# Kernel tuning notes

Measured on AMD Instinct MI355X. Metric: run time of the kernel, lower is better.

The kernel has to match this reference:

```python
import jax, jax.numpy as jnp
import numpy as np

N_NODES = 50000
N_EDGES = 800000
F_IN = 128
NUM_GRAPHS = 64
BN_EPS = 1e-5


def _graph_conv(x, src, dst, ew, Wl, bl, Wr, n_nodes):
    # PyG GraphConv: out = lin_l(aggr_add(x_j * w_e)) + lin_r(x)
    msg = x[src] * ew[:, None]                       # [E, F]
    agg = jax.ops.segment_sum(msg, dst, num_segments=n_nodes)  # [N, F]
    return agg @ Wl + bl + x @ Wr


def setup_inputs() -> dict:
    key = jax.random.key(0)
    ks = jax.random.split(key, 16)
    x = jax.random.normal(ks[0], (N_NODES, F_IN), dtype=jnp.float32)
    edge_index = jax.random.randint(ks[1], (2, N_EDGES), 0, N_NODES, dtype=jnp.int64)
    edge_attr = jax.random.uniform(ks[2], (N_EDGES,), dtype=jnp.float32)
    batch = jnp.sort(jax.random.randint(ks[3], (N_NODES,), 0, NUM_GRAPHS, dtype=jnp.int64))

    def lin(k, fin, fout):
        s = 1.0 / np.sqrt(fin)
        return jax.random.uniform(k, (fin, fout), jnp.float32, -s, s)

    params = {
        "Wl1": lin(ks[4], F_IN, 512), "bl1": jnp.zeros((512,), jnp.float32), "Wr1": lin(ks[5], F_IN, 512),
        "Wl2": lin(ks[6], 512, 512),  "bl2": jnp.zeros((512,), jnp.float32), "Wr2": lin(ks[7], 512, 512),
        "Wl3": lin(ks[8], 512, 256),  "bl3": jnp.zeros((256,), jnp.float32), "Wr3": lin(ks[9], 512, 256),
        "bn_gamma": jnp.ones((512,), jnp.float32), "bn_beta": jnp.zeros((512,), jnp.float32),
        "bn_mean": jnp.zeros((512,), jnp.float32),  "bn_var": jnp.ones((512,), jnp.float32),
        "W4": lin(ks[10], 256, 64), "b4": jnp.zeros((64,), jnp.float32),
        "W5": lin(ks[11], 64, 1),  "b5": jnp.zeros((1,), jnp.float32),
    }
    return {"x": x, "edge_index": edge_index, "edge_attr": edge_attr, "batch": batch, **params}


def reference(x, edge_index, edge_attr, batch,
              Wl1, bl1, Wr1, Wl2, bl2, Wr2, Wl3, bl3, Wr3,
              bn_gamma, bn_beta, bn_mean, bn_var,
              W4, b4, W5, b5):
    src, dst = edge_index[0], edge_index[1]
    n = x.shape[0]
    h = jax.nn.relu(_graph_conv(x, src, dst, edge_attr, Wl1, bl1, Wr1, n))
    h = _graph_conv(h, src, dst, edge_attr, Wl2, bl2, Wr2, n)
    # BatchNorm1d in eval mode (running stats)
    h = (h - bn_mean) * jax.lax.rsqrt(bn_var + BN_EPS) * bn_gamma + bn_beta
    h = jax.nn.relu(h)
    h = jax.nn.relu(_graph_conv(h, src, dst, edge_attr, Wl3, bl3, Wr3, n))
    # global mean pool
    sums = jax.ops.segment_sum(h, batch, num_segments=NUM_GRAPHS)           # [G, 256]
    cnts = jax.ops.segment_sum(jnp.ones((n,), h.dtype), batch, num_segments=NUM_GRAPHS)
    g = sums / jnp.maximum(cnts, 1.0)[:, None]
    # dropout is identity in eval mode
    g = jax.nn.relu(g @ W4 + b4)
    return jax.nn.relu(g @ W5 + b5)  # [G, 1]
```

## Files before the change

kernel.cpp:

```cpp
#include <hip/hip_runtime.h>

#define NN 50000
#define NE 800000
#define NG 64
#define BN_EPS 1e-5f

typedef unsigned short u16;
typedef unsigned int u32;
typedef unsigned char u8;
typedef long i64b;
struct alignas(8) us4 { u16 x, y, z, w; };
typedef float f32x4 __attribute__((ext_vector_type(4)));

__device__ inline int clampi(int v, int lo, int hi) {
  return v < lo ? lo : (v > hi ? hi : v);
}
__device__ inline float bf2f(u16 h) { return __uint_as_float((u32)h << 16); }
__device__ inline u16 f2bf_rne(float f) {
  u32 u = __float_as_uint(f);
  return (u16)((u + 0x7fff + ((u >> 16) & 1)) >> 16);
}
__device__ inline void gload_lds16(const void* g, void* l) {
  __builtin_amdgcn_global_load_lds(
      (const __attribute__((address_space(1))) u32*)g,
      (__attribute__((address_space(3))) u32*)l, 16, 0, 0);
}
__device__ inline float4 fp8x4f(u32 q) {
  float4 r;
  r.x = __builtin_amdgcn_cvt_f32_fp8(q, 0);
  r.y = __builtin_amdgcn_cvt_f32_fp8(q, 1);
  r.z = __builtin_amdgcn_cvt_f32_fp8(q, 2);
  r.w = __builtin_amdgcn_cvt_f32_fp8(q, 3);
  return r;
}
__device__ inline u32 f4fp8(float a, float b, float c, float d) {
  u32 p = __builtin_amdgcn_cvt_pk_fp8_f32(a, b, 0u, false);
  return __builtin_amdgcn_cvt_pk_fp8_f32(c, d, p, true);
}
__device__ inline u8 f2fp8(float v) {
  return (u8)(__builtin_amdgcn_cvt_pk_fp8_f32(v, 0.f, 0u, false) & 0xffu);
}

__global__ void k_zero32(u32* __restrict__ p, int n) {
  int i = blockIdx.x * 256 + threadIdx.x;
  if (i < n) p[i] = 0u;
}

__global__ void k_count(const int* __restrict__ dst, int* __restrict__ deg) {
  int e = blockIdx.x * 256 + threadIdx.x;
  if (e < NE) atomicAdd(&deg[clampi(dst[e], 0, NN - 1)], 1);
}

__global__ void k_scan_block(const int* __restrict__ deg, int* __restrict__ excl,
                             int* __restrict__ aux) {
  __shared__ int s[256];
  int t = threadIdx.x;
  int idx = blockIdx.x * 256 + t;
  int v = (idx < NN) ? deg[idx] : 0;
  s[t] = v;
  __syncthreads();
  for (int off = 1; off < 256; off <<= 1) {
    int x = (t >= off) ? s[t - off] : 0;
    __syncthreads();
    s[t] += x;
    __syncthreads();
  }
  if (idx < NN) excl[idx] = s[t] - v;
  if (t == 255) aux[blockIdx.x] = s[255];
}

__global__ void k_scan_aux(int* aux, int nblk) {
  __shared__ int s[256];
  int t = threadIdx.x;
  int v = (t < nblk) ? aux[t] : 0;
  s[t] = v;
  __syncthreads();
  for (int off = 1; off < 256; off <<= 1) {
    int x = (t >= off) ? s[t - off] : 0;
    __syncthreads();
    s[t] += x;
    __syncthreads();
  }
  if (t < nblk) aux[t] = s[t] - v;
}

__global__ void k_fix(int* __restrict__ rowptr, const int* __restrict__ aux,
                      int* __restrict__ cursor) {
  int idx = blockIdx.x * 256 + threadIdx.x;
  if (idx < NN) {
    int v = rowptr[idx] + aux[blockIdx.x];
    rowptr[idx] = v;
    cursor[idx] = v;
  }
  if (idx == 0) rowptr[NN] = NE;
}

__global__ void k_fill(const int* __restrict__ src, const int* __restrict__ dst,
                       const float* __restrict__ ew, int* __restrict__ cursor,
                       int* __restrict__ csr_src, float* __restrict__ csr_w) {
  int e = blockIdx.x * 256 + threadIdx.x;
  if (e < NE) {
    int d = clampi(dst[e], 0, NN - 1);
    int p = atomicAdd(&cursor[d], 1);
    p = clampi(p, 0, NE - 1);
    csr_src[p] = clampi(src[e], 0, NN - 1);
    csr_w[p] = ew[e];
  }
}

__global__ void k_prep(const float* __restrict__ x, u8* __restrict__ xf8,
                       const float* __restrict__ Wl1, const float* __restrict__ Wr1,
                       u8* __restrict__ t1,
                       const float* __restrict__ Wl2, const float* __restrict__ Wr2,
                       u8* __restrict__ t2,
                       const float* __restrict__ Wl3, const float* __restrict__ Wr3,
                       u8* __restrict__ t3) {
  int b = blockIdx.x, tid = threadIdx.x;
  if (b < 512) {
    int n = b, k = tid;
    float v = (k < 128) ? Wl1[(size_t)k * 512 + n] : Wr1[(size_t)(k - 128) * 512 + n];
    t1[(size_t)n * 256 + k] = f2fp8(v);
  } else if (b < 1024) {
    int n = b - 512;
    for (int k = tid; k < 1024; k += 256) {
      float v = (k < 512) ? Wl2[(size_t)k * 512 + n] : Wr2[(size_t)(k - 512) * 512 + n];
      t2[(size_t)n * 1024 + k] = f2fp8(v);
    }
  } else if (b < 1536) {
    int n = b - 1024;
    for (int k = tid; k < 512; k += 256) {
      float v = (n < 256) ? Wl3[(size_t)k * 256 + n] : Wr3[(size_t)k * 256 + (n - 256)];
      t3[(size_t)n * 512 + k] = f2fp8(v);
    }
  } else {
    int i = (b - 1536) * 256 + tid;
    if (i < NN * 128 / 8) {
      size_t o = (size_t)i * 8;
      float4 a = *(const float4*)(x + o);
      float4 c = *(const float4*)(x + o + 4);
      u32 p0 = f4fp8(a.x, a.y, a.z, a.w);
      u32 p1 = f4fp8(c.x, c.y, c.z, c.w);
      *(uint2*)(xf8 + o) = make_uint2(p0, p1);
    }
  }
}

__global__ void k_aggf512(const u8* __restrict__ xf8, const int* __restrict__ rowptr,
                          const int* __restrict__ csr_src, const float* __restrict__ csr_w,
                          u8* __restrict__ out) {
  int n = blockIdx.x;
  int t = threadIdx.x;
  int beg = rowptr[n], end = rowptr[n + 1];
  float4 acc = {0.f, 0.f, 0.f, 0.f};
  int e = beg;
  for (; e + 4 <= end; e += 4) {
    int s0 = csr_src[e], s1 = csr_src[e + 1];
    int s2 = csr_src[e + 2], s3 = csr_src[e + 3];
    float w0 = csr_w[e], w1 = csr_w[e + 1];
    float w2 = csr_w[e + 2], w3 = csr_w[e + 3];
    u32 q0 = *(const u32*)(xf8 + (size_t)s0 * 512 + t * 4);
    u32 q1 = *(const u32*)(xf8 + (size_t)s1 * 512 + t * 4);
    u32 q2 = *(const u32*)(xf8 + (size_t)s2 * 512 + t * 4);
    u32 q3 = *(const u32*)(xf8 + (size_t)s3 * 512 + t * 4);
    float4 v0 = fp8x4f(q0), v1 = fp8x4f(q1), v2 = fp8x4f(q2), v3 = fp8x4f(q3);
    acc.x += v0.x * w0 + v1.x * w1 + v2.x * w2 + v3.x * w3;
    acc.y += v0.y * w0 + v1.y * w1 + v2.y * w2 + v3.y * w3;
    acc.z += v0.z * w0 + v1.z * w1 + v2.z * w2 + v3.z * w3;
    acc.w += v0.w * w0 + v1.w * w1 + v2.w * w2 + v3.w * w3;
  }
  for (; e < end; ++e) {
    int s0 = csr_src[e];
    float w0 = csr_w[e];
    float4 v0 = fp8x4f(*(const u32*)(xf8 + (size_t)s0 * 512 + t * 4));
    acc.x += v0.x * w0; acc.y += v0.y * w0;
    acc.z += v0.z * w0; acc.w += v0.w * w0;
  }
  *(u32*)(out + (size_t)n * 512 + t * 4) = f4fp8(acc.x, acc.y, acc.z, acc.w);
}

__global__ void k_aggf128(const u8* __restrict__ xf8, const int* __restrict__ rowptr,
                          const int* __restrict__ csr_src, const float* __restrict__ csr_w,
                          u8* __restrict__ out) {
  int sub = threadIdx.x >> 5;
  int lane = threadIdx.x & 31;
  int n = blockIdx.x * 2 + sub;
  if (n >= NN) return;
  int beg = rowptr[n], end = rowptr[n + 1];
  float4 acc = {0.f, 0.f, 0.f, 0.f};
  int e = beg;
  for (; e + 2 <= end; e += 2) {
    int s0 = csr_src[e], s1 = csr_src[e + 1];
    float w0 = csr_w[e], w1 = csr_w[e + 1];
    float4 v0 = fp8x4f(*(const u32*)(xf8 + (size_t)s0 * 128 + lane * 4));
    float4 v1 = fp8x4f(*(const u32*)(xf8 + (size_t)s1 * 128 + lane * 4));
    acc.x += v0.x * w0 + v1.x * w1;
    acc.y += v0.y * w0 + v1.y * w1;
    acc.z += v0.z * w0 + v1.z * w1;
    acc.w += v0.w * w0 + v1.w * w1;
  }
  if (e < end) {
    int s0 = csr_src[e];
    float w0 = csr_w[e];
    float4 v0 = fp8x4f(*(const u32*)(xf8 + (size_t)s0 * 128 + lane * 4));
    acc.x += v0.x * w0; acc.y += v0.y * w0;
    acc.z += v0.z * w0; acc.w += v0.w * w0;
  }
  *(u32*)(out + (size_t)n * 128 + lane * 4) = f4fp8(acc.x, acc.y, acc.z, acc.w);
}

__global__ void k_aggcomb(const u8* __restrict__ P, const u8* __restrict__ Q,
                          const int* __restrict__ rowptr, const int* __restrict__ csr_src,
                          const float* __restrict__ csr_w,
                          const float* __restrict__ bl3, u16* __restrict__ h3) {
  int sub = threadIdx.x >> 6;
  int lane = threadIdx.x & 63;
  int n = blockIdx.x * 2 + sub;
  if (n >= NN) return;
  int beg = rowptr[n], end = rowptr[n + 1];
  float4 acc = {0.f, 0.f, 0.f, 0.f};
  int e = beg;
  for (; e + 4 <= end; e += 4) {
    int s0 = csr_src[e], s1 = csr_src[e + 1];
    int s2 = csr_src[e + 2], s3 = csr_src[e + 3];
    float w0 = csr_w[e], w1 = csr_w[e + 1];
    float w2 = csr_w[e + 2], w3 = csr_w[e + 3];
    float4 v0 = fp8x4f(*(const u32*)(P + (size_t)s0 * 256 + lane * 4));
    float4 v1 = fp8x4f(*(const u32*)(P + (size_t)s1 * 256 + lane * 4));
    float4 v2 = fp8x4f(*(const u32*)(P + (size_t)s2 * 256 + lane * 4));
    float4 v3 = fp8x4f(*(const u32*)(P + (size_t)s3 * 256 + lane * 4));
    acc.x += v0.x * w0 + v1.x * w1 + v2.x * w2 + v3.x * w3;
    acc.y += v0.y * w0 + v1.y * w1 + v2.y * w2 + v3.y * w3;
    acc.z += v0.z * w0 + v1.z * w1 + v2.z * w2 + v3.z * w3;
    acc.w += v0.w * w0 + v1.w * w1 + v2.w * w2 + v3.w * w3;
  }
  for (; e < end; ++e) {
    int s0 = csr_src[e];
    float w0 = csr_w[e];
    float4 v0 = fp8x4f(*(const u32*)(P + (size_t)s0 * 256 + lane * 4));
    acc.x += v0.x * w0; acc.y += v0.y * w0;
    acc.z += v0.z * w0; acc.w += v0.w * w0;
  }
  float4 qv = fp8x4f(*(const u32*)(Q + (size_t)n * 256 + lane * 4));
  float4 bb = *(const float4*)(bl3 + lane * 4);
  us4 o;
  o.x = f2bf_rne(fmaxf(acc.x + qv.x + bb.x, 0.f));
  o.y = f2bf_rne(fmaxf(acc.y + qv.y + bb.y, 0.f));
  o.z = f2bf_rne(fmaxf(acc.z + qv.z + bb.z, 0.f));
  o.w = f2bf_rne(fmaxf(acc.w + qv.w + bb.w, 0.f));
  *(us4*)(h3 + (size_t)n * 256 + lane * 4) = o;
}

template <int K, int W0, int EPI>
__global__ __launch_bounds__(256) void k_gemm(
    const u8* __restrict__ A0, const u8* __restrict__ A1,
    const u8* __restrict__ Wt, const float* __restrict__ bias,
    const float* __restrict__ gamma, const float* __restrict__ beta,
    const float* __restrict__ mean, const float* __restrict__ var,
    u8* __restrict__ O8g, u8* __restrict__ O8b) {
  constexpr int FOUT = 512;
  __shared__ char LDSC[32768];
  u8* AS = (u8*)LDSC;
  u8* BS = (u8*)(LDSC + 16384);
  int tid = threadIdx.x;
  int wid = tid >> 6, l = tid & 63;
  int wr = wid >> 1, wc = wid & 1;

  int nwg = gridDim.x;
  int q8 = nwg >> 3, r8 = nwg & 7;
  int xcd = blockIdx.x & 7, idx = blockIdx.x >> 3;
  int L = (xcd < r8 ? xcd * (q8 + 1) : r8 * (q8 + 1) + (xcd - r8) * q8) + idx;
  int n0 = (L >> 2) * 128, c0 = (L & 3) * 128;

  f32x4 acc[4][4] = {};

  int srw = 32 * wid + (l >> 3);
  int sch = l & 7;

  for (int k0 = 0; k0 < K; k0 += 128) {
    __syncthreads();
    {
      const u8* s; int rs; int seg;
      if (k0 < W0) { s = A0; rs = W0; seg = k0; }
      else         { s = A1; rs = K - W0; seg = k0 - W0; }
#pragma unroll
      for (int j = 0; j < 4; ++j) {
        int r = srw + 8 * j;
        int gr = n0 + r;
        if (gr >= NN) gr = NN - 1;
        int cc = sch ^ (r & 7);
        gload_lds16(s + (size_t)gr * rs + seg + cc * 16, AS + (32 * wid + 8 * j) * 128);
      }
#pragma unroll
      for (int j = 0; j < 4; ++j) {
        int r = srw + 8 * j;
        int cc = sch ^ (r & 7);
        gload_lds16(Wt + (size_t)(c0 + r) * K + k0 + cc * 16, BS + (32 * wid + 8 * j) * 128);
      }
    }
    __syncthreads();

#pragma unroll
    for (int ks = 0; ks < 4; ++ks) {
      i64b b[4];
#pragma unroll
      for (int n = 0; n < 4; ++n) {
        int col = wc * 64 + n * 16 + (l & 15);
        int byte = (col * 128 + ks * 32 + ((l >> 4) << 3)) ^ ((col & 7) << 4);
        b[n] = *(const i64b*)((const char*)BS + byte);
      }
#pragma unroll
      for (int m = 0; m < 4; ++m) {
        int row = wr * 64 + m * 16 + (l & 15);
        int byte = (row * 128 + ks * 32 + ((l >> 4) << 3)) ^ ((row & 7) << 4);
        i64b a = *(const i64b*)((const char*)AS + byte);
#pragma unroll
        for (int n = 0; n < 4; ++n)
          acc[m][n] = __builtin_amdgcn_mfma_f32_16x16x32_fp8_fp8(a, b[n], acc[m][n], 0, 0, 0);
      }
    }
  }

  __syncthreads();
  u8* O8 = (u8*)LDSC;
#pragma unroll
  for (int n = 0; n < 4; ++n) {
    int colL = wc * 64 + n * 16 + (l & 15);
    int col = c0 + colL;
    float bs = (EPI == 2) ? 0.f : bias[col];
    float sc = 1.f, sf = 0.f;
    if (EPI == 1) {
      sc = rsqrtf(var[col] + BN_EPS) * gamma[col];
      sf = beta[col] - mean[col] * sc;
    }
#pragma unroll
    for (int m = 0; m < 4; ++m) {
      int rowL0 = wr * 64 + m * 16 + ((l >> 4) << 2);
#pragma unroll
      for (int r = 0; r < 4; ++r) {
        float v = acc[m][n][r];
        if (EPI != 2) {
          v += bs;
          if (EPI == 1) v = v * sc + sf;
          v = fmaxf(v, 0.f);
        }
        int rowL = rowL0 + r;
        int byte = (rowL * 128 + colL) ^ ((rowL & 7) << 4);
        O8[byte] = f2fp8(v);
      }
    }
  }
  __syncthreads();
#pragma unroll
  for (int i = 0; i < 4; ++i) {
    int chunk = i * 256 + tid;
    int rowL = chunk >> 3;
    int cs = (chunk & 7) * 16;
    int rr = n0 + rowL;
    if (rr < NN) {
      int byte = (rowL * 128 + cs) ^ ((rowL & 7) << 4);
      uint4 val = *(const uint4*)((const char*)O8 + byte);
      if (EPI == 2) {
        u8* dstp = (c0 < 256) ? O8g : O8b;
        int cc0 = (c0 < 256) ? c0 : c0 - 256;
        *(uint4*)(dstp + (size_t)rr * 256 + cc0 + cs) = val;
      } else {
        *(uint4*)(O8g + (size_t)rr * FOUT + c0 + cs) = val;
      }
    }
  }
}

__global__ void k_counts(const int* __restrict__ batch, float* __restrict__ cnt) {
  int g = threadIdx.x;
  int lo = 0, hi = NN;
  while (lo < hi) { int m = (lo + hi) >> 1; if (batch[m] < g) lo = m + 1; else hi = m; }
  int a = lo;
  lo = 0; hi = NN;
  int g1 = g + 1;
  while (lo < hi) { int m = (lo + hi) >> 1; if (batch[m] < g1) lo = m + 1; else hi = m; }
  cnt[g] = (float)(lo - a);
}

__global__ void k_pool(const u16* __restrict__ h, const int* __restrict__ batch,
                       float* __restrict__ sums) {
  int f = threadIdx.x;
  int n0 = blockIdx.x * 128;
  int n1 = n0 + 128; if (n1 > NN) n1 = NN;
  float acc = 0.f;
  int cur = clampi(batch[n0], 0, NG - 1);
  for (int n = n0; n < n1; ++n) {
    int g = clampi(batch[n], 0, NG - 1);
    if (g != cur) {
      atomicAdd(&sums[(size_t)cur * 256 + f], acc);
      acc = 0.f;
      cur = g;
    }
    acc += bf2f(h[(size_t)n * 256 + f]);
  }
  atomicAdd(&sums[(size_t)cur * 256 + f], acc);
}

__global__ void k_mlp(const float* __restrict__ sums, const float* __restrict__ cnt,
                      const float* __restrict__ W4, const float* __restrict__ b4,
                      const float* __restrict__ W5, const float* __restrict__ b5,
                      float* __restrict__ out) {
  __shared__ float g[256];
  int b = blockIdx.x, t = threadIdx.x;
  float inv = 1.f / fmaxf(cnt[b], 1.f);
#pragma unroll
  for (int q = 0; q < 4; ++q) g[q * 64 + t] = sums[(size_t)b * 256 + q * 64 + t] * inv;
  __syncthreads();
  float acc = 0.f;
#pragma unroll 8
  for (int k = 0; k < 256; ++k) acc += g[k] * W4[k * 64 + t];
  float a = fmaxf(acc + b4[t], 0.f) * W5[t];
  for (int off = 32; off; off >>= 1) a += __shfl_down(a, off, 64);
  if (t == 0) out[b] = fmaxf(a + b5[0], 0.f);
}

extern "C" void kernel_launch(void* const* d_in, const int* in_sizes, int n_in,
                              void* d_out, int out_size, void* d_ws, size_t ws_size,
                              hipStream_t stream) {
  const float* x     = (const float*)d_in[0];
  const int*   eidx  = (const int*)d_in[1];
  const float* ew    = (const float*)d_in[2];
  const int*   batch = (const int*)d_in[3];
  const float* Wl1 = (const float*)d_in[4];
  const float* bl1 = (const float*)d_in[5];
  const float* Wr1 = (const float*)d_in[6];
  const float* Wl2 = (const float*)d_in[7];
  const float* bl2 = (const float*)d_in[8];
  const float* Wr2 = (const float*)d_in[9];
  const float* Wl3 = (const float*)d_in[10];
  const float* bl3 = (const float*)d_in[11];
  const float* Wr3 = (const float*)d_in[12];
  const float* gamma = (const float*)d_in[13];
  const float* beta  = (const float*)d_in[14];
  const float* mean  = (const float*)d_in[15];
  const float* var   = (const float*)d_in[16];
  const float* W4 = (const float*)d_in[17];
  const float* b4 = (const float*)d_in[18];
  const float* W5 = (const float*)d_in[19];
  const float* b5 = (const float*)d_in[20];

  const int* src = eidx;
  const int* dst = eidx + NE;

  const size_t P8 = (size_t)NN * 512;
  char* w = (char*)d_ws;
  u8*  X1f8 = (u8*)w; w += P8;
  u8*  X2f8 = (u8*)w; w += P8;
  u8*  Agf8 = (u8*)w; w += P8;
  u8*  Xf8  = (u8*)w; w += (size_t)NN * 128;
  u16* h3 = (u16*)w; w += (size_t)NN * 256 * 2;
  u8* Wt1 = (u8*)w; w += (size_t)512 * 256;
  u8* Wt2 = (u8*)w; w += (size_t)512 * 1024;
  u8* Wt3 = (u8*)w; w += (size_t)512 * 512;
  int*   csr_src = (int*)w;   w += (size_t)NE * 4;
  float* csr_w   = (float*)w; w += (size_t)NE * 4;
  int*   rowptr  = (int*)w;   w += ((size_t)NN + 4) * 4;
  int*   cursor  = (int*)w;   w += (size_t)NN * 4;
  int*   aux     = (int*)w;   w += 1024;
  float* sums    = (float*)w; w += (size_t)NG * 256 * 4;
  float* cnt     = (float*)w; w += 1024;
  u8* Pf8 = Agf8;
  u8* Qf8 = Agf8 + (size_t)NN * 256;

  int nblk = (NN + 255) / 256;

  k_zero32<<<nblk, 256, 0, stream>>>((u32*)cursor, NN);
  k_count<<<(NE + 255) / 256, 256, 0, stream>>>(dst, cursor);
  k_scan_block<<<nblk, 256, 0, stream>>>(cursor, rowptr, aux);
  k_scan_aux<<<1, 256, 0, stream>>>(aux, nblk);
  k_fix<<<nblk, 256, 0, stream>>>(rowptr, aux, cursor);
  k_fill<<<(NE + 255) / 256, 256, 0, stream>>>(src, dst, ew, cursor, csr_src, csr_w);
  k_prep<<<1536 + (NN * 128 / 8 + 255) / 256, 256, 0, stream>>>(
      x, Xf8, Wl1, Wr1, Wt1, Wl2, Wr2, Wt2, Wl3, Wr3, Wt3);

  const int NWG = 391 * 4;

  k_aggf128<<<(NN + 1) / 2, 64, 0, stream>>>(Xf8, rowptr, csr_src, csr_w, Agf8);
  k_gemm<256, 128, 0><<<NWG, 256, 0, stream>>>(
      Agf8, Xf8, Wt1, bl1, nullptr, nullptr, nullptr, nullptr, X1f8, nullptr);

  k_aggf512<<<NN, 128, 0, stream>>>(X1f8, rowptr, csr_src, csr_w, Agf8);
  k_gemm<1024, 512, 1><<<NWG, 256, 0, stream>>>(
      Agf8, X1f8, Wt2, bl2, gamma, beta, mean, var, X2f8, nullptr);

  k_gemm<512, 512, 2><<<NWG, 256, 0, stream>>>(
      X2f8, X2f8, Wt3, nullptr, nullptr, nullptr, nullptr, nullptr, Pf8, Qf8);
  k_aggcomb<<<(NN + 1) / 2, 128, 0, stream>>>(Pf8, Qf8, rowptr, csr_src, csr_w, bl3, h3);

  k_zero32<<<(NG * 256 + 255) / 256, 256, 0, stream>>>((u32*)sums, NG * 256);
  k_pool<<<(NN + 127) / 128, 256, 0, stream>>>(h3, batch, sums);
  k_counts<<<1, 64, 0, stream>>>(batch, cnt);
  k_mlp<<<NG, 64, 0, stream>>>(sums, cnt, W4, b4, W5, b5, (float*)d_out);
}
```

Measured before the change: 402.7 us.

## Fuse pooling, counts and MLP; pack two nodes per aggf512 block; unroll aggf128

Replaces the zero, pool, count and MLP kernels with one fused kernel, one block per graph. Each block binary-searches its node range, sums the h3 rows in a serial loop, then runs the small MLP. This removes three launches and the atomics. k_aggf512 now handles two nodes per 256-thread block, and k_aggf128 unrolls its edge loop by four for more loads in flight. The risk is that only 64 blocks each walk about 780 rows serially, so the pooling step may become latency-bound with little parallelism.

```diff
diff --git a/kernel.cpp b/kernel.cpp
--- a/kernel.cpp
+++ b/kernel.cpp
@@ -148,8 +148,10 @@
 __global__ void k_aggf512(const u8* __restrict__ xf8, const int* __restrict__ rowptr,
                           const int* __restrict__ csr_src, const float* __restrict__ csr_w,
                           u8* __restrict__ out) {
-  int n = blockIdx.x;
-  int t = threadIdx.x;
+  int sub = threadIdx.x >> 7;
+  int t = threadIdx.x & 127;
+  int n = blockIdx.x * 2 + sub;
+  if (n >= NN) return;
   int beg = rowptr[n], end = rowptr[n + 1];
   float4 acc = {0.f, 0.f, 0.f, 0.f};
   int e = beg;
@@ -188,17 +190,21 @@
   int beg = rowptr[n], end = rowptr[n + 1];
   float4 acc = {0.f, 0.f, 0.f, 0.f};
   int e = beg;
-  for (; e + 2 <= end; e += 2) {
+  for (; e + 4 <= end; e += 4) {
     int s0 = csr_src[e], s1 = csr_src[e + 1];
+    int s2 = csr_src[e + 2], s3 = csr_src[e + 3];
     float w0 = csr_w[e], w1 = csr_w[e + 1];
+    float w2 = csr_w[e + 2], w3 = csr_w[e + 3];
     float4 v0 = fp8x4f(*(const u32*)(xf8 + (size_t)s0 * 128 + lane * 4));
     float4 v1 = fp8x4f(*(const u32*)(xf8 + (size_t)s1 * 128 + lane * 4));
-    acc.x += v0.x * w0 + v1.x * w1;
-    acc.y += v0.y * w0 + v1.y * w1;
-    acc.z += v0.z * w0 + v1.z * w1;
-    acc.w += v0.w * w0 + v1.w * w1;
-  }
-  if (e < end) {
+    float4 v2 = fp8x4f(*(const u32*)(xf8 + (size_t)s2 * 128 + lane * 4));
+    float4 v3 = fp8x4f(*(const u32*)(xf8 + (size_t)s3 * 128 + lane * 4));
+    acc.x += v0.x * w0 + v1.x * w1 + v2.x * w2 + v3.x * w3;
+    acc.y += v0.y * w0 + v1.y * w1 + v2.y * w2 + v3.y * w3;
+    acc.z += v0.z * w0 + v1.z * w1 + v2.z * w2 + v3.z * w3;
+    acc.w += v0.w * w0 + v1.w * w1 + v2.w * w2 + v3.w * w3;
+  }
+  for (; e < end; ++e) {
     int s0 = csr_src[e];
     float w0 = csr_w[e];
     float4 v0 = fp8x4f(*(const u32*)(xf8 + (size_t)s0 * 128 + lane * 4));
@@ -370,52 +376,31 @@
   }
 }
 
-__global__ void k_counts(const int* __restrict__ batch, float* __restrict__ cnt) {
-  int g = threadIdx.x;
-  int lo = 0, hi = NN;
-  while (lo < hi) { int m = (lo + hi) >> 1; if (batch[m] < g) lo = m + 1; else hi = m; }
-  int a = lo;
-  lo = 0; hi = NN;
-  int g1 = g + 1;
-  while (lo < hi) { int m = (lo + hi) >> 1; if (batch[m] < g1) lo = m + 1; else hi = m; }
-  cnt[g] = (float)(lo - a);
-}
-
-__global__ void k_pool(const u16* __restrict__ h, const int* __restrict__ batch,
-                       float* __restrict__ sums) {
-  int f = threadIdx.x;
-  int n0 = blockIdx.x * 128;
-  int n1 = n0 + 128; if (n1 > NN) n1 = NN;
-  float acc = 0.f;
-  int cur = clampi(batch[n0], 0, NG - 1);
-  for (int n = n0; n < n1; ++n) {
-    int g = clampi(batch[n], 0, NG - 1);
-    if (g != cur) {
-      atomicAdd(&sums[(size_t)cur * 256 + f], acc);
-      acc = 0.f;
-      cur = g;
-    }
-    acc += bf2f(h[(size_t)n * 256 + f]);
-  }
-  atomicAdd(&sums[(size_t)cur * 256 + f], acc);
-}
-
-__global__ void k_mlp(const float* __restrict__ sums, const float* __restrict__ cnt,
-                      const float* __restrict__ W4, const float* __restrict__ b4,
-                      const float* __restrict__ W5, const float* __restrict__ b5,
-                      float* __restrict__ out) {
+__global__ void k_poolmlp(const u16* __restrict__ h3, const int* __restrict__ batch,
+                          const float* __restrict__ W4, const float* __restrict__ b4,
+                          const float* __restrict__ W5, const float* __restrict__ b5,
+                          float* __restrict__ out) {
   __shared__ float g[256];
   int b = blockIdx.x, t = threadIdx.x;
-  float inv = 1.f / fmaxf(cnt[b], 1.f);
-#pragma unroll
-  for (int q = 0; q < 4; ++q) g[q * 64 + t] = sums[(size_t)b * 256 + q * 64 + t] * inv;
+  int lo = 0, hi = NN;
+  while (lo < hi) { int m = (lo + hi) >> 1; if (batch[m] < b) lo = m + 1; else hi = m; }
+  int a0 = lo;
+  lo = 0; hi = NN;
+  int b1 = b + 1;
+  while (lo < hi) { int m = (lo + hi) >> 1; if (batch[m] < b1) lo = m + 1; else hi = m; }
+  int a1 = lo;
+  float acc = 0.f;
+  for (int n = a0; n < a1; ++n) acc += bf2f(h3[(size_t)n * 256 + t]);
+  g[t] = acc / fmaxf((float)(a1 - a0), 1.f);
   __syncthreads();
-  float acc = 0.f;
+  if (t < 64) {
+    float s = 0.f;
 #pragma unroll 8
-  for (int k = 0; k < 256; ++k) acc += g[k] * W4[k * 64 + t];
-  float a = fmaxf(acc + b4[t], 0.f) * W5[t];
-  for (int off = 32; off; off >>= 1) a += __shfl_down(a, off, 64);
-  if (t == 0) out[b] = fmaxf(a + b5[0], 0.f);
+    for (int k = 0; k < 256; ++k) s += g[k] * W4[k * 64 + t];
+    float a = fmaxf(s + b4[t], 0.f) * W5[t];
+    for (int off = 32; off; off >>= 1) a += __shfl_down(a, off, 64);
+    if (t == 0) out[b] = fmaxf(a + b5[0], 0.f);
+  }
 }
 
 extern "C" void kernel_launch(void* const* d_in, const int* in_sizes, int n_in,
@@ -461,8 +446,6 @@
   int*   rowptr  = (int*)w;   w += ((size_t)NN + 4) * 4;
   int*   cursor  = (int*)w;   w += (size_t)NN * 4;
   int*   aux     = (int*)w;   w += 1024;
-  float* sums    = (float*)w; w += (size_t)NG * 256 * 4;
-  float* cnt     = (float*)w; w += 1024;
   u8* Pf8 = Agf8;
   u8* Qf8 = Agf8 + (size_t)NN * 256;
 
@@ -483,7 +466,7 @@
   k_gemm<256, 128, 0><<<NWG, 256, 0, stream>>>(
       Agf8, Xf8, Wt1, bl1, nullptr, nullptr, nullptr, nullptr, X1f8, nullptr);
 
-  k_aggf512<<<NN, 128, 0, stream>>>(X1f8, rowptr, csr_src, csr_w, Agf8);
+  k_aggf512<<<(NN + 1) / 2, 256, 0, stream>>>(X1f8, rowptr, csr_src, csr_w, Agf8);
   k_gemm<1024, 512, 1><<<NWG, 256, 0, stream>>>(
       Agf8, X1f8, Wt2, bl2, gamma, beta, mean, var, X2f8, nullptr);
 
@@ -491,8 +474,5 @@
       X2f8, X2f8, Wt3, nullptr, nullptr, nullptr, nullptr, nullptr, Pf8, Qf8);
   k_aggcomb<<<(NN + 1) / 2, 128, 0, stream>>>(Pf8, Qf8, rowptr, csr_src, csr_w, bl3, h3);
 
-  k_zero32<<<(NG * 256 + 255) / 256, 256, 0, stream>>>((u32*)sums, NG * 256);
-  k_pool<<<(NN + 127) / 128, 256, 0, stream>>>(h3, batch, sums);
-  k_counts<<<1, 64, 0, stream>>>(batch, cnt);
-  k_mlp<<<NG, 64, 0, stream>>>(sums, cnt, W4, b4, W5, b5, (float*)d_out);
-}
+  k_poolmlp<<<NG, 256, 0, stream>>>(h3, batch, W4, b4, W5, b5, (float*)d_out);
+}
```

Result: slower. 548.4 us (+36.2%).
